# Performance work log

Hardware: AMD Instinct MI355X
Metric: run time of the kernel (lower is better)

## Reference

```python
import jax, jax.numpy as jnp
import numpy as np

N = 50000      # nodes
E = 800000     # edges (avg degree 16)
F0 = 3         # node feature dim
EF = 3         # edge feature dim
C = 4          # num classes


def _lin_params(k, din, dout):
    k1, k2 = jax.random.split(k)
    s = 1.0 / np.sqrt(din)
    W = jax.random.uniform(k1, (dout, din), jnp.float32, -s, s)
    b = jax.random.uniform(k2, (dout,), jnp.float32, -s, s)
    return W, b


def setup_inputs() -> dict:
    key = jax.random.key(0)
    ks = jax.random.split(key, 8)
    x = jax.random.normal(ks[0], (N, F0), jnp.float32)
    edge_index = jax.random.randint(ks[1], (2, E), 0, N, jnp.int32)
    edge_attr = jax.random.uniform(ks[2], (E, EF), dtype=jnp.float32)
    W1, b1 = _lin_params(ks[3], 2 * F0 + EF, 128)
    W2, b2 = _lin_params(ks[4], 2 * 128 + EF, 64)
    W3, b3 = _lin_params(ks[5], 2 * 64 + EF, 32)
    Wc, bc = _lin_params(ks[6], 32, C)
    return dict(x=x, edge_index=edge_index, edge_attr=edge_attr,
                W1=W1, b1=b1, W2=W2, b2=b2, W3=W3, b3=b3, Wc=Wc, bc=bc)


def _edgeconv(x, src, dst, ea, W, b, n):
    # message = Linear(cat([x_i, x_j, edge_attr])); aggregated by scatter-add to dst (x_i side).
    # Split W so the node-side matmuls happen once per node instead of per edge.
    f = x.shape[1]
    Wi, Wj, We = W[:, :f], W[:, f:2 * f], W[:, 2 * f:]
    ai = x @ Wi.T   # [N, out]
    aj = x @ Wj.T   # [N, out]
    msg = ai[dst] + aj[src] + ea @ We.T + b  # [E_aug, out]
    return jax.ops.segment_sum(msg, dst, num_segments=n)


def reference(x, edge_index, edge_attr, W1, b1, W2, b2, W3, b3, Wc, bc):
    n = x.shape[0]
    loops = jnp.arange(n, dtype=edge_index.dtype)
    src = jnp.concatenate([edge_index[0], loops])  # x_j indices
    dst = jnp.concatenate([edge_index[1], loops])  # x_i indices (aggregation targets)
    ea = jnp.concatenate([edge_attr, jnp.zeros((n, edge_attr.shape[1]), edge_attr.dtype)])
    h = jax.nn.relu(_edgeconv(x, src, dst, ea, W1, b1, n))
    h = jax.nn.relu(_edgeconv(h, src, dst, ea, W2, b2, n))
    h = _edgeconv(h, src, dst, ea, W3, b3, n)  # no relu after conv3 in the original
    logits = h @ Wc.T + bc
    return jax.nn.log_softmax(logits, axis=1)
```

## Files before the change

### kernel.cpp

```cpp
#include <hip/hip_runtime.h>
#include <math.h>


static inline size_t align256(size_t x) { return (x + 255) & ~size_t(255); }

typedef unsigned short ushort_t;
using frag8  = __attribute__((ext_vector_type(8))) short;
using f32x4v = __attribute__((ext_vector_type(4))) float;
using half8  = __attribute__((ext_vector_type(8))) _Float16;

__device__ inline unsigned short f2bf(float f) {
    unsigned u = __float_as_uint(f);
    unsigned r = (u + 0x7fffu + ((u >> 16) & 1u)) >> 16;
    return (unsigned short)r;
}
__device__ inline float bflo(unsigned u) { return __uint_as_float(u << 16); }
__device__ inline float bfhi(unsigned u) { return __uint_as_float(u & 0xffff0000u); }


__global__ __launch_bounds__(256) void prep(
    const int* __restrict__ ei, int* __restrict__ count,
    int* __restrict__ pos, int E,
    const float* __restrict__ x, float4* __restrict__ xpad, int n,
    const float* __restrict__ W2, ushort_t* __restrict__ W2bf,
    const float* __restrict__ W3, const float* __restrict__ b3,
    const float* __restrict__ Wc, const float* __restrict__ bc,
    float* __restrict__ AB, float* __restrict__ consts,
    int eb4, int nxb)
{
    const int t = threadIdx.x;
    const int b = blockIdx.x;
    if (b < eb4) {
        int e4 = (b * 256 + t) * 4;
        if (e4 >= E) return;
        if (e4 + 3 < E) {
            int4 d = *(const int4*)(ei + E + e4);
            int4 po;
            po.x = atomicAdd(&count[d.x], 1);
            po.y = atomicAdd(&count[d.y], 1);
            po.z = atomicAdd(&count[d.z], 1);
            po.w = atomicAdd(&count[d.w], 1);
            *(int4*)(pos + e4) = po;
        } else {
            for (int e = e4; e < E; ++e)
                pos[e] = atomicAdd(&count[ei[E + e]], 1);
        }
    } else if (b < eb4 + nxb) {
        int j = (b - eb4) * 256 + t;
        if (j < n) {
            const float* xp = x + (size_t)j * 3;
            xpad[j] = make_float4(xp[0], xp[1], xp[2], 0.f);
        }
    } else if (b < eb4 + nxb + 4) {
        int wb = b - (eb4 + nxb);
        int i0 = wb * 4096 + t;
        int i1 = (wb + 1) * 4096;
        for (int idx = i0; idx < i1; idx += 256) {
            int jg = idx >> 7, k = idx & 127;
            float w = (jg < 64) ? W2[jg * 259 + k] : W2[(jg - 64) * 259 + 128 + k];
            W2bf[idx] = f2bf(w);
        }
    } else {
        for (int idx = t; idx < 512; idx += 256) {
            int j = idx >> 6, k = idx & 63;
            int jj = j & 3;
            int base = (j >= 4) ? 64 : 0;
            float s = 0.f;
            #pragma unroll
            for (int c = 0; c < 32; ++c)
                s += Wc[jj * 32 + c] * W3[c * 131 + base + k];
            AB[idx] = s;
        }
        if (t < 4) {
            float db = 0.f;
            for (int c = 0; c < 32; ++c) db += Wc[t * 32 + c] * b3[c];
            consts[t] = db;
            consts[4 + t] = bc[t];
            for (int q = 0; q < 3; ++q) {
                float s = 0.f;
                for (int c = 0; c < 32; ++c) s += Wc[t * 32 + c] * W3[c * 131 + 128 + q];
                consts[8 + t * 3 + q] = s;
            }
        }
    }
}


__global__ __launch_bounds__(256) void scan_pass1(
    const int* __restrict__ count, int* __restrict__ rowstart,
    int* __restrict__ bsum, int n)
{
    __shared__ int sh[256];
    const int tid = threadIdx.x;
    const int base = blockIdx.x * 1024 + tid * 4;
    int v0 = 0, v1 = 0, v2 = 0, v3 = 0;
    if (base + 3 < n) {
        int4 c = *(const int4*)(count + base);
        v0 = c.x; v1 = c.y; v2 = c.z; v3 = c.w;
    } else {
        if (base + 0 < n) v0 = count[base + 0];
        if (base + 1 < n) v1 = count[base + 1];
        if (base + 2 < n) v2 = count[base + 2];
        if (base + 3 < n) v3 = count[base + 3];
    }
    int tsum = v0 + v1 + v2 + v3;
    sh[tid] = tsum;
    __syncthreads();
    for (int off = 1; off < 256; off <<= 1) {
        int t = (tid >= off) ? sh[tid - off] : 0;
        __syncthreads();
        sh[tid] += t;
        __syncthreads();
    }
    int excl = sh[tid] - tsum;
    int p0 = excl + v0, p1 = p0 + v1, p2 = p1 + v2, p3 = p2 + v3;
    if (base + 0 < n) rowstart[base + 1] = p0;
    if (base + 1 < n) rowstart[base + 2] = p1;
    if (base + 2 < n) rowstart[base + 3] = p2;
    if (base + 3 < n) rowstart[base + 4] = p3;
    if (tid == 255) bsum[blockIdx.x] = sh[255];
}


__global__ __launch_bounds__(256) void csr_scatter2(
    const int* __restrict__ ei, const float* __restrict__ ea,
    const int* __restrict__ pos, const int* __restrict__ rowstart,
    const int* __restrict__ bsum, int nb,
    uint2* __restrict__ csrp, int* __restrict__ rowfin,
    int E, int n, int eb4)
{
    __shared__ int sBex[64];
    const int tid = threadIdx.x;
    if (tid < 64) {
        int v = (tid < nb) ? bsum[tid] : 0;
        int xx = v;
        #pragma unroll
        for (int off = 1; off < 64; off <<= 1) {
            int t = __shfl_up(xx, off);
            if (tid >= off) xx += t;
        }
        sBex[tid] = xx - v;
    }
    __syncthreads();

    if (blockIdx.x < eb4) {
        int e4 = (blockIdx.x * 256 + tid) * 4;
        if (e4 >= E) return;
        if (e4 + 3 < E) {
            int4 s = *(const int4*)(ei + e4);
            int4 d = *(const int4*)(ei + E + e4);
            int4 po = *(const int4*)(pos + e4);
            float4 a = *(const float4*)(ea + (size_t)e4 * 3);
            float4 bq = *(const float4*)(ea + (size_t)e4 * 3 + 4);
            float4 c = *(const float4*)(ea + (size_t)e4 * 3 + 8);
            float ev[12] = { a.x, a.y, a.z, a.w, bq.x, bq.y, bq.z, bq.w, c.x, c.y, c.z, c.w };
            int sv[4] = { s.x, s.y, s.z, s.w };
            int dv[4] = { d.x, d.y, d.z, d.w };
            int pv[4] = { po.x, po.y, po.z, po.w };
            #pragma unroll
            for (int r = 0; r < 4; ++r) {
                uint2 p;
                p.x = (unsigned)f2bf(ev[r * 3 + 0]) | ((unsigned)f2bf(ev[r * 3 + 1]) << 16);
                p.y = (unsigned)f2bf(ev[r * 3 + 2]) | ((unsigned)sv[r] << 16);
                int dd = dv[r];
                int rs = (dd == 0) ? 0 : (rowstart[dd] + sBex[(dd - 1) >> 10]);
                csrp[rs + pv[r]] = p;
            }
        } else {
            for (int e = e4; e < E; ++e) {
                uint2 p;
                p.x = (unsigned)f2bf(ea[e * 3 + 0]) | ((unsigned)f2bf(ea[e * 3 + 1]) << 16);
                p.y = (unsigned)f2bf(ea[e * 3 + 2]) | ((unsigned)ei[e] << 16);
                int dd = ei[E + e];
                int rs = (dd == 0) ? 0 : (rowstart[dd] + sBex[(dd - 1) >> 10]);
                csrp[rs + pos[e]] = p;
            }
        }
    } else {
        int j = (blockIdx.x - eb4) * 256 + tid;
        if (j <= n)
            rowfin[j] = (j == 0) ? 0 : (rowstart[j] + sBex[(j - 1) >> 10]);
    }
}


__global__ __launch_bounds__(128) void h1_gemm(
    const float4* __restrict__ xpad, const float* __restrict__ W1,
    const float* __restrict__ b1, const float* __restrict__ b2,
    const int* __restrict__ rowstart,
    const uint2* __restrict__ csrp, float4* __restrict__ eagg4,
    const ushort_t* __restrict__ W2bf,
    float* __restrict__ AI2, _Float16* __restrict__ AJ2, int n_nodes)
{
    constexpr int HS = 152;
    __shared__ float sM[10 * 128];
    __shared__ ushort_t sH[32 * HS];

    const int tid = threadIdx.x;
    for (int t = tid; t < 1280; t += 128) {
        int k = t >> 7, c = t & 127;
        int cp = (c & 15) * 8 + (c >> 4);
        sM[k * 128 + cp] = (k < 9) ? W1[c * 9 + k] : b1[c];
    }
    __syncthreads();

    const int base = blockIdx.x * 32;
    const int wave = tid >> 6, wl = tid & 63;
    const int grp = wl >> 3, ch8 = wl & 7;

    #pragma unroll
    for (int pass = 0; pass < 2; ++pass) {
        int nl = pass * 16 + wave * 8 + grp;
        int n = base + nl;
        float hv[16];
        if (n < n_nodes) {
            int s0 = rowstart[n], s1 = rowstart[n + 1];
            float xx = 0.f, xy = 0.f, xz = 0.f, ex = 0.f, ey = 0.f, ez = 0.f;
            int i = s0 + ch8;
            for (; i + 8 < s1; i += 16) {
                uint2 p0 = csrp[i];
                uint2 p1 = csrp[i + 8];
                float4 xv0 = xpad[(int)(p0.y >> 16)];
                float4 xv1 = xpad[(int)(p1.y >> 16)];
                ex += bflo(p0.x) + bflo(p1.x);
                ey += bfhi(p0.x) + bfhi(p1.x);
                ez += bflo(p0.y) + bflo(p1.y);
                xx += xv0.x + xv1.x; xy += xv0.y + xv1.y; xz += xv0.z + xv1.z;
            }
            if (i < s1) {
                uint2 p0 = csrp[i];
                float4 xv0 = xpad[(int)(p0.y >> 16)];
                ex += bflo(p0.x); ey += bfhi(p0.x); ez += bflo(p0.y);
                xx += xv0.x; xy += xv0.y; xz += xv0.z;
            }
            #pragma unroll
            for (int off = 1; off < 8; off <<= 1) {
                xx += __shfl_xor(xx, off); xy += __shfl_xor(xy, off); xz += __shfl_xor(xz, off);
                ex += __shfl_xor(ex, off); ey += __shfl_xor(ey, off); ez += __shfl_xor(ez, off);
            }
            float deg = (float)(s1 - s0 + 1);
            float4 xs = xpad[n];
            float v[10] = { deg * xs.x, deg * xs.y, deg * xs.z,
                            xs.x + xx, xs.y + xy, xs.z + xz,
                            ex, ey, ez, deg };
            #pragma unroll
            for (int q = 0; q < 16; ++q) {
                float h = 0.f;
                #pragma unroll
                for (int k = 0; k < 10; ++k) h += v[k] * sM[k * 128 + q * 8 + ch8];
                hv[q] = fmaxf(h, 0.f);
            }
            if (ch8 == 0) eagg4[n] = make_float4(ex, ey, ez, 0.f);
        } else {
            #pragma unroll
            for (int q = 0; q < 16; ++q) hv[q] = 0.f;
        }
        #pragma unroll
        for (int g = 0; g < 2; ++g) {
            uint4 u;
            u.x = (unsigned)f2bf(hv[g * 8 + 0]) | ((unsigned)f2bf(hv[g * 8 + 1]) << 16);
            u.y = (unsigned)f2bf(hv[g * 8 + 2]) | ((unsigned)f2bf(hv[g * 8 + 3]) << 16);
            u.z = (unsigned)f2bf(hv[g * 8 + 4]) | ((unsigned)f2bf(hv[g * 8 + 5]) << 16);
            u.w = (unsigned)f2bf(hv[g * 8 + 6]) | ((unsigned)f2bf(hv[g * 8 + 7]) << 16);
            *(uint4*)(sH + nl * HS + ch8 * 16 + g * 8) = u;
        }
    }
    __syncthreads();

    const int m = wl & 15, quad = wl >> 4;

    frag8 a[4];
    #pragma unroll
    for (int ks = 0; ks < 4; ++ks)
        a[ks] = *(const frag8*)(sH + (wave * 16 + m) * HS + ks * 32 + quad * 8);

    f32x4v acc[8];
    #pragma unroll
    for (int t = 0; t < 8; ++t) acc[t] = (f32x4v)(0.f);

    #pragma unroll
    for (int t = 0; t < 8; ++t) {
        #pragma unroll
        for (int ks = 0; ks < 4; ++ks) {
            frag8 b = *(const frag8*)(W2bf + (t * 16 + m) * 128 + ks * 32 + quad * 8);
            acc[t] = __builtin_amdgcn_mfma_f32_16x16x32_bf16(a[ks], b, acc[t], 0, 0, 0);
        }
    }

    float b2v[4];
    #pragma unroll
    for (int t = 0; t < 4; ++t) b2v[t] = b2[t * 16 + m];

    #pragma unroll
    for (int reg = 0; reg < 4; ++reg) {
        int grow = base + wave * 16 + quad * 4 + reg;
        if (grow >= n_nodes) continue;
        #pragma unroll
        for (int t = 0; t < 4; ++t)
            AI2[(size_t)grow * 64 + t * 16 + m] = acc[t][reg] + b2v[t];
        #pragma unroll
        for (int t = 4; t < 8; ++t)
            AJ2[(size_t)grow * 64 + (t - 4) * 16 + m] = (_Float16)acc[t][reg];
    }
}


__global__ __launch_bounds__(256) void gather2(
    const float* __restrict__ AI2, const _Float16* __restrict__ AJ2,
    const float* __restrict__ W2,
    const float4* __restrict__ eagg4, const int* __restrict__ rowstart,
    const uint2* __restrict__ csrp, const float* __restrict__ AB,
    float* __restrict__ U, float* __restrict__ Z, int n_nodes)
{
    __shared__ float sAB[512];
    __shared__ float sWe[192];
    const int tid = threadIdx.x;
    for (int t = tid; t < 512; t += 256) sAB[t] = AB[t];
    for (int t = tid; t < 192; t += 256) {
        int c = t / 3, q = t % 3;
        sWe[t] = W2[c * 259 + 256 + q];
    }
    __syncthreads();

    int wl = tid & 63;
    int grp = wl >> 3, ch8 = wl & 7;
    int n = blockIdx.x * 32 + (tid >> 6) * 8 + grp;
    if (n >= n_nodes) return;

    int s0 = rowstart[n], s1 = rowstart[n + 1];

    half8 hacc0 = (half8)(_Float16)0.f;
    half8 hacc1 = (half8)(_Float16)0.f;
    for (int base = s0; base < s1; base += 8) {
        int j = base + ch8;
        if (j >= s1) j = s1 - 1;
        int myidx = (int)(csrp[j].y >> 16);
        int cnt = s1 - base; if (cnt > 8) cnt = 8;
        #pragma unroll
        for (int k = 0; k < 8; ++k) {
            int s = __shfl(myidx, grp * 8 + k);
            if (k < cnt) {
                half8 v = *(const half8*)(AJ2 + (size_t)s * 64 + ch8 * 8);
                if (k & 1) hacc1 += v; else hacc0 += v;
            }
        }
    }
    float acc[8];
    #pragma unroll
    for (int q = 0; q < 8; ++q) acc[q] = (float)hacc0[q] + (float)hacc1[q];

    float deg = (float)(s1 - s0 + 1);
    float4 e4 = eagg4[n];
    const float* aip = AI2 + (size_t)n * 64 + ch8 * 8;
    float4 aiA = *(const float4*)(aip);
    float4 aiB = *(const float4*)(aip + 4);
    half8 su = *(const half8*)(AJ2 + (size_t)n * 64 + ch8 * 8);
    float av[8] = { aiA.x, aiA.y, aiA.z, aiA.w, aiB.x, aiB.y, aiB.z, aiB.w };
    float r[8];
    #pragma unroll
    for (int q = 0; q < 8; ++q) {
        int c = ch8 * 8 + q;
        float we = sWe[c * 3] * e4.x + sWe[c * 3 + 1] * e4.y + sWe[c * 3 + 2] * e4.z;
        r[q] = fmaxf(deg * av[q] + (float)su[q] + we + acc[q], 0.f);
    }
    float pj[8];
    #pragma unroll
    for (int j = 0; j < 8; ++j) {
        float4 wA = *(const float4*)(sAB + j * 64 + ch8 * 8);
        float4 wB = *(const float4*)(sAB + j * 64 + ch8 * 8 + 4);
        pj[j] = r[0] * wA.x + r[1] * wA.y + r[2] * wA.z + r[3] * wA.w
              + r[4] * wB.x + r[5] * wB.y + r[6] * wB.z + r[7] * wB.w;
    }
    #pragma unroll
    for (int off = 1; off < 8; off <<= 1)
        #pragma unroll
        for (int j = 0; j < 8; ++j) pj[j] += __shfl_xor(pj[j], off);

    if (ch8 == 0) {
        *(float4*)(U + (size_t)n * 4) = make_float4(pj[0], pj[1], pj[2], pj[3]);
        *(float4*)(Z + (size_t)n * 4) = make_float4(pj[4], pj[5], pj[6], pj[7]);
    }
}


__global__ __launch_bounds__(256) void final_softmax(
    const float* __restrict__ U, const float* __restrict__ Z,
    const float4* __restrict__ eagg4, const int* __restrict__ rowstart,
    const uint2* __restrict__ csrp, const float* __restrict__ consts,
    float* __restrict__ out, int n_nodes)
{
    int wl = threadIdx.x & 63;
    int grp = wl >> 3, ch8 = wl & 7;
    int n = blockIdx.x * 32 + (threadIdx.x >> 6) * 8 + grp;
    if (n >= n_nodes) return;

    int s0 = rowstart[n], s1 = rowstart[n + 1];
    float ax = 0.f, ay = 0.f, az = 0.f, aw = 0.f;
    for (int i = s0 + ch8; i < s1; i += 8) {
        int s = (int)(csrp[i].y >> 16);
        float4 z = *(const float4*)(Z + (size_t)s * 4);
        ax += z.x; ay += z.y; az += z.z; aw += z.w;
    }
    #pragma unroll
    for (int off = 1; off < 8; off <<= 1) {
        ax += __shfl_xor(ax, off); ay += __shfl_xor(ay, off);
        az += __shfl_xor(az, off); aw += __shfl_xor(aw, off);
    }
    if (ch8 != 0) return;

    float deg = (float)(s1 - s0 + 1);
    float4 u = *(const float4*)(U + (size_t)n * 4);
    float4 zs = *(const float4*)(Z + (size_t)n * 4);
    float4 e4 = eagg4[n];
    float av[4] = { ax + zs.x, ay + zs.y, az + zs.z, aw + zs.w };
    float uv[4] = { u.x, u.y, u.z, u.w };
    float lg[4];
    #pragma unroll
    for (int j = 0; j < 4; ++j) {
        lg[j] = deg * (uv[j] + consts[j]) + av[j] + consts[4 + j]
              + consts[8 + j * 3] * e4.x + consts[9 + j * 3] * e4.y
              + consts[10 + j * 3] * e4.z;
    }
    float m = fmaxf(fmaxf(lg[0], lg[1]), fmaxf(lg[2], lg[3]));
    float lse = logf(expf(lg[0] - m) + expf(lg[1] - m) + expf(lg[2] - m) + expf(lg[3] - m));
    *(float4*)(out + (size_t)n * 4) =
        make_float4(lg[0] - m - lse, lg[1] - m - lse, lg[2] - m - lse, lg[3] - m - lse);
}


extern "C" void kernel_launch(void* const* d_in, const int* in_sizes, int n_in,
                              void* d_out, int out_size, void* d_ws, size_t ws_size,
                              hipStream_t stream)
{
    const float* x    = (const float*)d_in[0];
    const int*   ei   = (const int*)  d_in[1];
    const float* ea   = (const float*)d_in[2];
    const float* W1   = (const float*)d_in[3];
    const float* b1   = (const float*)d_in[4];
    const float* W2   = (const float*)d_in[5];
    const float* b2   = (const float*)d_in[6];
    const float* W3   = (const float*)d_in[7];
    const float* b3   = (const float*)d_in[8];
    const float* Wc   = (const float*)d_in[9];
    const float* bc   = (const float*)d_in[10];
    float* out = (float*)d_out;

    const int N = in_sizes[0] / 3;
    const int E = in_sizes[1] / 2;

    char* ws = (char*)d_ws;
    size_t off = 0;
    int*    count    = (int*)(ws + off);            off = align256(off + (size_t)N * 4);
    int*    pos      = (int*)(ws + off);            off = align256(off + (size_t)E * 4);
    int*    rowstart = (int*)(ws + off);            off = align256(off + (size_t)(N + 1) * 4);
    int*    rowfin   = (int*)(ws + off);            off = align256(off + (size_t)(N + 1) * 4);
    uint2*  csrp     = (uint2*)(ws + off);          off = align256(off + (size_t)E * 8);
    int*    bsum     = (int*)(ws + off);            off = align256(off + 256);
    float*  AB       = (float*)(ws + off);          off = align256(off + 512 * 4);
    float*  consts   = (float*)(ws + off);          off = align256(off + 32 * 4);
    ushort_t* W2bf   = (ushort_t*)(ws + off);       off = align256(off + 128 * 128 * 2);
    float4* xpad     = (float4*)(ws + off);         off = align256(off + (size_t)N * 16);
    float4* eagg4    = (float4*)(ws + off);         off = align256(off + (size_t)N * 16);
    float*  AI2      = (float*)(ws + off);          off = align256(off + (size_t)N * 64 * 4);
    _Float16* AJ2    = (_Float16*)(ws + off);       off = align256(off + (size_t)N * 64 * 2);
    float*  Ubuf     = (float*)(ws + off);          off = align256(off + (size_t)N * 16);
    float*  Zbuf     = (float*)(ws + off);          off = align256(off + (size_t)N * 16);
    (void)ws_size;

    hipMemsetAsync(count, 0, (size_t)N * 4, stream);

    const int eb4 = ((E + 3) / 4 + 255) / 256;
    const int nxb = (N + 255) / 256;
    const int nb1 = (N + 1023) / 1024;
    const int nfb = (N + 1 + 255) / 256;

    prep<<<eb4 + nxb + 5, 256, 0, stream>>>(ei, count, pos, E,
                                            x, xpad, N, W2, W2bf,
                                            W3, b3, Wc, bc, AB, consts,
                                            eb4, nxb);

    scan_pass1<<<nb1, 256, 0, stream>>>(count, rowstart, bsum, N);

    csr_scatter2<<<eb4 + nfb, 256, 0, stream>>>(ei, ea, pos, rowstart, bsum, nb1,
                                                csrp, rowfin, E, N, eb4);

    h1_gemm<<<(N + 31) / 32, 128, 0, stream>>>(xpad, W1, b1, b2, rowfin, csrp,
                                               eagg4, W2bf, AI2, AJ2, N);

    const int gb = (N + 31) / 32;
    gather2<<<gb, 256, 0, stream>>>(AI2, AJ2, W2, eagg4, rowfin, csrp, AB, Ubuf, Zbuf, N);

    final_softmax<<<gb, 256, 0, stream>>>(Ubuf, Zbuf, eagg4, rowfin, csrp, consts, out, N);
}
```

Baseline: 199.7 us.

## Store AI2 as fp16, stage h1_gemm outputs in LDS for coalesced stores

Doubles the h1_gemm block to 256 threads and 64 nodes. AI2 changes from fp32 to fp16, which halves its memory traffic. The MFMA results are staged through shared memory so each row goes out as 16-byte coalesced writes instead of scattered 2/4-byte stores, and gather2 reads AI2 as a half8. The costs are lower precision in AI2, which is multiplied by degree before the ReLU, plus larger LDS use and extra barriers.

```diff
diff --git a/kernel.cpp b/kernel.cpp
--- a/kernel.cpp
+++ b/kernel.cpp
@@ -16,6 +16,12 @@
 }
 __device__ inline float bflo(unsigned u) { return __uint_as_float(u << 16); }
 __device__ inline float bfhi(unsigned u) { return __uint_as_float(u & 0xffff0000u); }
+__device__ inline ushort_t f2hbits(float f) {
+    _Float16 h = (_Float16)f;
+    ushort_t u;
+    __builtin_memcpy(&u, &h, 2);
+    return u;
+}
 
 
 __global__ __launch_bounds__(256) void prep(
@@ -184,33 +190,34 @@
 }
 
 
-__global__ __launch_bounds__(128) void h1_gemm(
+__global__ __launch_bounds__(256) void h1_gemm(
     const float4* __restrict__ xpad, const float* __restrict__ W1,
     const float* __restrict__ b1, const float* __restrict__ b2,
     const int* __restrict__ rowstart,
     const uint2* __restrict__ csrp, float4* __restrict__ eagg4,
     const ushort_t* __restrict__ W2bf,
-    float* __restrict__ AI2, _Float16* __restrict__ AJ2, int n_nodes)
+    _Float16* __restrict__ AI2, _Float16* __restrict__ AJ2, int n_nodes)
 {
     constexpr int HS = 152;
+    constexpr int OS = 72;
     __shared__ float sM[10 * 128];
-    __shared__ ushort_t sH[32 * HS];
+    __shared__ ushort_t sH[64 * HS];
 
     const int tid = threadIdx.x;
-    for (int t = tid; t < 1280; t += 128) {
+    for (int t = tid; t < 1280; t += 256) {
         int k = t >> 7, c = t & 127;
         int cp = (c & 15) * 8 + (c >> 4);
         sM[k * 128 + cp] = (k < 9) ? W1[c * 9 + k] : b1[c];
     }
     __syncthreads();
 
-    const int base = blockIdx.x * 32;
+    const int base = blockIdx.x * 64;
     const int wave = tid >> 6, wl = tid & 63;
     const int grp = wl >> 3, ch8 = wl & 7;
 
     #pragma unroll
     for (int pass = 0; pass < 2; ++pass) {
-        int nl = pass * 16 + wave * 8 + grp;
+        int nl = pass * 32 + wave * 8 + grp;
         int n = base + nl;
         float hv[16];
         if (n < n_nodes) {
@@ -291,22 +298,37 @@
     #pragma unroll
     for (int t = 0; t < 4; ++t) b2v[t] = b2[t * 16 + m];
 
+    __syncthreads();
+    ushort_t* sAI = sH;
+    ushort_t* sAJ = sH + 64 * OS;
+
     #pragma unroll
     for (int reg = 0; reg < 4; ++reg) {
-        int grow = base + wave * 16 + quad * 4 + reg;
-        if (grow >= n_nodes) continue;
+        int rl = wave * 16 + quad * 4 + reg;
         #pragma unroll
         for (int t = 0; t < 4; ++t)
-            AI2[(size_t)grow * 64 + t * 16 + m] = acc[t][reg] + b2v[t];
+            sAI[rl * OS + t * 16 + m] = f2hbits(acc[t][reg] + b2v[t]);
         #pragma unroll
         for (int t = 4; t < 8; ++t)
-            AJ2[(size_t)grow * 64 + (t - 4) * 16 + m] = (_Float16)acc[t][reg];
+            sAJ[rl * OS + (t - 4) * 16 + m] = f2hbits(acc[t][reg]);
+    }
+    __syncthreads();
+
+    for (int idx = tid; idx < 512; idx += 256) {
+        int row = idx >> 3, seg = idx & 7;
+        int grow = base + row;
+        if (grow < n_nodes) {
+            *(uint4*)((ushort_t*)AI2 + (size_t)grow * 64 + seg * 8) =
+                *(const uint4*)(sAI + row * OS + seg * 8);
+            *(uint4*)((ushort_t*)AJ2 + (size_t)grow * 64 + seg * 8) =
+                *(const uint4*)(sAJ + row * OS + seg * 8);
+        }
     }
 }
 
 
 __global__ __launch_bounds__(256) void gather2(
-    const float* __restrict__ AI2, const _Float16* __restrict__ AJ2,
+    const _Float16* __restrict__ AI2, const _Float16* __restrict__ AJ2,
     const float* __restrict__ W2,
     const float4* __restrict__ eagg4, const int* __restrict__ rowstart,
     const uint2* __restrict__ csrp, const float* __restrict__ AB,
@@ -351,17 +373,14 @@
 
     float deg = (float)(s1 - s0 + 1);
     float4 e4 = eagg4[n];
-    const float* aip = AI2 + (size_t)n * 64 + ch8 * 8;
-    float4 aiA = *(const float4*)(aip);
-    float4 aiB = *(const float4*)(aip + 4);
+    half8 ai = *(const half8*)(AI2 + (size_t)n * 64 + ch8 * 8);
     half8 su = *(const half8*)(AJ2 + (size_t)n * 64 + ch8 * 8);
-    float av[8] = { aiA.x, aiA.y, aiA.z, aiA.w, aiB.x, aiB.y, aiB.z, aiB.w };
     float r[8];
     #pragma unroll
     for (int q = 0; q < 8; ++q) {
         int c = ch8 * 8 + q;
         float we = sWe[c * 3] * e4.x + sWe[c * 3 + 1] * e4.y + sWe[c * 3 + 2] * e4.z;
-        r[q] = fmaxf(deg * av[q] + (float)su[q] + we + acc[q], 0.f);
+        r[q] = fmaxf(deg * (float)ai[q] + (float)su[q] + we + acc[q], 0.f);
     }
     float pj[8];
     #pragma unroll
@@ -461,7 +480,7 @@
     ushort_t* W2bf   = (ushort_t*)(ws + off);       off = align256(off + 128 * 128 * 2);
     float4* xpad     = (float4*)(ws + off);         off = align256(off + (size_t)N * 16);
     float4* eagg4    = (float4*)(ws + off);         off = align256(off + (size_t)N * 16);
-    float*  AI2      = (float*)(ws + off);          off = align256(off + (size_t)N * 64 * 4);
+    _Float16* AI2    = (_Float16*)(ws + off);       off = align256(off + (size_t)N * 64 * 2);
     _Float16* AJ2    = (_Float16*)(ws + off);       off = align256(off + (size_t)N * 64 * 2);
     float*  Ubuf     = (float*)(ws + off);          off = align256(off + (size_t)N * 16);
     float*  Zbuf     = (float*)(ws + off);          off = align256(off + (size_t)N * 16);
@@ -484,7 +503,7 @@
     csr_scatter2<<<eb4 + nfb, 256, 0, stream>>>(ei, ea, pos, rowstart, bsum, nb1,
                                                 csrp, rowfin, E, N, eb4);
 
-    h1_gemm<<<(N + 31) / 32, 128, 0, stream>>>(xpad, W1, b1, b2, rowfin, csrp,
+    h1_gemm<<<(N + 63) / 64, 256, 0, stream>>>(xpad, W1, b1, b2, rowfin, csrp,
                                                eagg4, W2bf, AI2, AJ2, N);
 
     const int gb = (N + 31) / 32;
```

Result: no change. 196.7 us (-1.5%).
